# Kernel optimization log

Hardware: AMD Instinct MI355X
Metric: run time of the kernel (lower is better)

The kernel has to match this reference:

```python
import jax, jax.numpy as jnp
import numpy as np

N_NODES = 100000
N_EDGES = 1600000
D_IN = 128
HIDDEN = 128
EPS = 1e-5


def setup_inputs() -> dict:
    key = jax.random.key(0)
    ks = jax.random.split(key, 12)
    glorot = lambda k, o, i: jax.random.normal(k, (o, i), jnp.float32) * (2.0 / (o + i)) ** 0.5
    return {
        "x": jax.random.normal(ks[0], (N_NODES, D_IN), jnp.float32),
        "edge_index": jax.random.randint(ks[1], (2, N_EDGES), 0, N_NODES, jnp.int64),
        # SAGEConv layer 1: lin_l (neighbors, with bias), lin_r (root, no bias)
        "Wl1": glorot(ks[2], HIDDEN, D_IN),
        "bl1": jnp.zeros((HIDDEN,), jnp.float32),
        "Wr1": glorot(ks[3], HIDDEN, D_IN),
        # SAGEConv layer 2
        "Wl2": glorot(ks[4], HIDDEN, HIDDEN),
        "bl2": jnp.zeros((HIDDEN,), jnp.float32),
        "Wr2": glorot(ks[5], HIDDEN, HIDDEN),
        # BatchNorm1d affine params
        "gamma": jnp.ones((HIDDEN,), jnp.float32),
        "beta": jnp.zeros((HIDDEN,), jnp.float32),
        # final fc (xavier_uniform weight, zero bias per init_weights)
        "fcW": jax.random.uniform(ks[6], (HIDDEN, HIDDEN), jnp.float32, -1.0, 1.0) * (6.0 / (2 * HIDDEN)) ** 0.5,
        "fcb": jnp.zeros((HIDDEN,), jnp.float32),
    }


def _sage_conv(h, src, dst, n, Wl, bl, Wr):
    # mean-aggregate neighbor features: scatter x[src] onto dst
    msg_sum = jax.ops.segment_sum(h[src], dst, num_segments=n)          # [N, F]
    deg = jax.ops.segment_sum(jnp.ones((src.shape[0],), h.dtype), dst, num_segments=n)
    agg = msg_sum / jnp.maximum(deg, 1.0)[:, None]
    return agg @ Wl.T + bl + h @ Wr.T


def reference(x, edge_index, Wl1, bl1, Wr1, Wl2, bl2, Wr2, gamma, beta, fcW, fcb):
    src, dst = edge_index[0], edge_index[1]
    n = x.shape[0]
    h = jax.nn.relu(_sage_conv(x, src, dst, n, Wl1, bl1, Wr1))  # inter-layer relu in PyG BasicGNN
    h = _sage_conv(h, src, dst, n, Wl2, bl2, Wr2)
    h = jax.nn.relu(h)
    # BatchNorm1d, training-mode (batch stats, biased variance)
    mu = h.mean(axis=0)
    var = ((h - mu) ** 2).mean(axis=0)
    h = (h - mu) * jax.lax.rsqrt(var + EPS) * gamma + beta
    # dropout p=0.0 -> identity
    return h @ fcW.T + fcb
```

## Files before the change

### kernel.cpp

```cpp
#include <hip/hip_runtime.h>
#include <hip/hip_bf16.h>

#define D 128
#define EPSV 1e-5f
#define BSH 7
#define BWIDTH 128
#define NCB 256
#define MAXBUCK 1024

typedef __attribute__((ext_vector_type(8))) short bf16x8;
typedef __attribute__((ext_vector_type(4))) float f32x4;
typedef unsigned short u16;

__device__ inline u16 f2bf(float f) {
    unsigned int u = __builtin_bit_cast(unsigned int, f);
    return (u16)((u + 0x7fffu + ((u >> 16) & 1u)) >> 16);
}
__device__ inline float bf2f(u16 u) {
    unsigned int x = ((unsigned int)u) << 16;
    return __builtin_bit_cast(float, x);
}

__global__ void k_cvt(const float* __restrict__ in, u16* __restrict__ out, long long n8) {
    long long i = (long long)blockIdx.x * blockDim.x + threadIdx.x;
    long long stride = (long long)gridDim.x * blockDim.x;
    for (; i < n8; i += stride) {
        const float4 v0 = *(const float4*)(in + i * 8);
        const float4 v1 = *(const float4*)(in + i * 8 + 4);
        bf16x8 o;
        o[0] = (short)f2bf(v0.x); o[1] = (short)f2bf(v0.y);
        o[2] = (short)f2bf(v0.z); o[3] = (short)f2bf(v0.w);
        o[4] = (short)f2bf(v1.x); o[5] = (short)f2bf(v1.y);
        o[6] = (short)f2bf(v1.z); o[7] = (short)f2bf(v1.w);
        *(bf16x8*)(out + i * 8) = o;
    }
}

__global__ __launch_bounds__(256) void k_bhist(const int* __restrict__ dst, int E, int chunk,
                                               int nbuck, int* __restrict__ bh) {
    __shared__ int h[MAXBUCK];
    int t = threadIdx.x;
    for (int i = t; i < nbuck; i += 256) h[i] = 0;
    __syncthreads();
    int beg = blockIdx.x * chunk, end = min(E, beg + chunk);
    for (int i = beg + t; i < end; i += 256) atomicAdd(&h[dst[i] >> BSH], 1);
    __syncthreads();
    for (int i = t; i < nbuck; i += 256) bh[(size_t)blockIdx.x * nbuck + i] = h[i];
}

__global__ __launch_bounds__(NCB) void k_colscan(int* __restrict__ bh, int nbuck, int* __restrict__ btot) {
    __shared__ int sm[NCB];
    int b = blockIdx.x;
    int t = threadIdx.x;
    int v = bh[(size_t)t * nbuck + b];
    sm[t] = v;
    __syncthreads();
    for (int off = 1; off < NCB; off <<= 1) {
        int a = (t >= off) ? sm[t - off] : 0;
        __syncthreads();
        sm[t] += a;
        __syncthreads();
    }
    bh[(size_t)t * nbuck + b] = sm[t] - v;
    if (t == NCB - 1) btot[b] = sm[t];
}

__global__ __launch_bounds__(1024) void k_btotscan(const int* __restrict__ btot, int nbuck,
                                                   int* __restrict__ bbase, int* __restrict__ row_ptr,
                                                   int M, int E) {
    __shared__ int sm[1024];
    int t = threadIdx.x;
    int v = (t < nbuck) ? btot[t] : 0;
    sm[t] = v;
    __syncthreads();
    for (int off = 1; off < 1024; off <<= 1) {
        int a = (t >= off) ? sm[t - off] : 0;
        __syncthreads();
        sm[t] += a;
        __syncthreads();
    }
    if (t < nbuck) bbase[t] = sm[t] - v;
    if (t == 0) { bbase[nbuck] = E; row_ptr[M] = E; }
}

__global__ __launch_bounds__(256) void k_bfill(const int* __restrict__ src, const int* __restrict__ dst,
                                               int E, int chunk, int nbuck, const int* __restrict__ bh,
                                               const int* __restrict__ bbase, unsigned int* __restrict__ pairs) {
    __shared__ int cur[MAXBUCK];
    int t = threadIdx.x;
    for (int i = t; i < nbuck; i += 256)
        cur[i] = bbase[i] + bh[(size_t)blockIdx.x * nbuck + i];
    __syncthreads();
    int beg = blockIdx.x * chunk, end = min(E, beg + chunk);
    for (int i = beg + t; i < end; i += 256) {
        int d = dst[i];
        int bk = d >> BSH;
        int pos = atomicAdd(&cur[bk], 1);
        pairs[pos] = (unsigned int)src[i] | ((unsigned int)(d & (BWIDTH - 1)) << 24);
    }
}

__global__ __launch_bounds__(256) void k_b2csr(const unsigned int* __restrict__ pairs,
                                               const int* __restrict__ bbase, int nbuck, int M,
                                               int* __restrict__ row_ptr, int* __restrict__ csr) {
    __shared__ int nh[BWIDTH];
    __shared__ int sc[BWIDTH];
    __shared__ int nc[BWIDTH];
    int b = blockIdx.x;
    int t = threadIdx.x;
    int node0 = b << BSH;
    int beg = bbase[b], end = bbase[b + 1];
    if (t < BWIDTH) nh[t] = 0;
    __syncthreads();
    for (int i = beg + t; i < end; i += 256) atomicAdd(&nh[pairs[i] >> 24], 1);
    __syncthreads();
    if (t < BWIDTH) sc[t] = nh[t];
    __syncthreads();
    for (int off = 1; off < BWIDTH; off <<= 1) {
        int a = 0;
        if (t < BWIDTH && t >= off) a = sc[t - off];
        __syncthreads();
        if (t < BWIDTH) sc[t] += a;
        __syncthreads();
    }
    if (t < BWIDTH) {
        int ex = sc[t] - nh[t];
        nc[t] = ex;
        int node = node0 + t;
        if (node < M) row_ptr[node] = beg + ex;
    }
    __syncthreads();
    for (int i = beg + t; i < end; i += 256) {
        unsigned int p = pairs[i];
        int pos = atomicAdd(&nc[p >> 24], 1);
        csr[beg + pos] = (int)(p & 0xFFFFFFu);
    }
}

__global__ __launch_bounds__(256) void k_gather(const u16* __restrict__ feat, const int* __restrict__ rp,
                                                const int* __restrict__ csr, u16* __restrict__ msg, int M) {
    int sub = threadIdx.x & 15;
    int node = blockIdx.x * 16 + (threadIdx.x >> 4);
    if (node >= M) return;
    int beg = rp[node], end = rp[node + 1];
    float a0[8], a1[8];
    #pragma unroll
    for (int j = 0; j < 8; j++) { a0[j] = 0.f; a1[j] = 0.f; }
    int e = beg;
    for (; e + 1 < end; e += 2) {
        int s0 = csr[e], s1 = csr[e + 1];
        bf16x8 v0 = *(const bf16x8*)(feat + (size_t)s0 * D + sub * 8);
        bf16x8 v1 = *(const bf16x8*)(feat + (size_t)s1 * D + sub * 8);
        #pragma unroll
        for (int j = 0; j < 8; j++) {
            a0[j] += bf2f((u16)v0[j]);
            a1[j] += bf2f((u16)v1[j]);
        }
    }
    if (e < end) {
        bf16x8 v0 = *(const bf16x8*)(feat + (size_t)csr[e] * D + sub * 8);
        #pragma unroll
        for (int j = 0; j < 8; j++) a0[j] += bf2f((u16)v0[j]);
    }
    float inv = 1.0f / fmaxf((float)(end - beg), 1.0f);
    bf16x8 o;
    #pragma unroll
    for (int j = 0; j < 8; j++) o[j] = (short)f2bf((a0[j] + a1[j]) * inv);
    *(bf16x8*)(msg + (size_t)node * D + sub * 8) = o;
}

template <int TWO, int RELU, int OUTBF>
__global__ __launch_bounds__(256) void k_gemm(
    const u16* __restrict__ A1, const u16* __restrict__ A2,
    const u16* __restrict__ W1b, const u16* __restrict__ W2b,
    const float* __restrict__ bias, void* __restrict__ Cout, int M) {
    int lane = threadIdx.x & 63;
    int wave = threadIdx.x >> 6;
    int rlo = lane & 15;
    int k0 = (lane >> 4) * 8;
    int m0 = blockIdx.x * 128 + wave * 32;

    f32x4 acc[2][8];
    #pragma unroll
    for (int mt = 0; mt < 2; mt++)
        #pragma unroll
        for (int nt = 0; nt < 8; nt++) acc[mt][nt] = (f32x4){0.f, 0.f, 0.f, 0.f};

    {
        bf16x8 af[2][4];
        #pragma unroll
        for (int mt = 0; mt < 2; mt++) {
            int ra = m0 + mt * 16 + rlo;
            if (ra > M - 1) ra = M - 1;
            const u16* arow = A1 + (size_t)ra * D;
            #pragma unroll
            for (int kk = 0; kk < 4; kk++)
                af[mt][kk] = *(const bf16x8*)(arow + kk * 32 + k0);
        }
        #pragma unroll
        for (int nt = 0; nt < 8; nt++) {
            const u16* wrow = W1b + (size_t)(nt * 16 + rlo) * D;
            bf16x8 wf[4];
            #pragma unroll
            for (int kk = 0; kk < 4; kk++)
                wf[kk] = *(const bf16x8*)(wrow + kk * 32 + k0);
            #pragma unroll
            for (int mt = 0; mt < 2; mt++)
                #pragma unroll
                for (int kk = 0; kk < 4; kk++)
                    acc[mt][nt] = __builtin_amdgcn_mfma_f32_16x16x32_bf16(af[mt][kk], wf[kk], acc[mt][nt], 0, 0, 0);
        }
    }

    if (TWO) {
        bf16x8 af[2][4];
        #pragma unroll
        for (int mt = 0; mt < 2; mt++) {
            int ra = m0 + mt * 16 + rlo;
            if (ra > M - 1) ra = M - 1;
            const u16* arow = A2 + (size_t)ra * D;
            #pragma unroll
            for (int kk = 0; kk < 4; kk++)
                af[mt][kk] = *(const bf16x8*)(arow + kk * 32 + k0);
        }
        #pragma unroll
        for (int nt = 0; nt < 8; nt++) {
            const u16* wrow = W2b + (size_t)(nt * 16 + rlo) * D;
            bf16x8 wf[4];
            #pragma unroll
            for (int kk = 0; kk < 4; kk++)
                wf[kk] = *(const bf16x8*)(wrow + kk * 32 + k0);
            #pragma unroll
            for (int mt = 0; mt < 2; mt++)
                #pragma unroll
                for (int kk = 0; kk < 4; kk++)
                    acc[mt][nt] = __builtin_amdgcn_mfma_f32_16x16x32_bf16(af[mt][kk], wf[kk], acc[mt][nt], 0, 0, 0);
        }
    }

    #pragma unroll
    for (int mt = 0; mt < 2; mt++)
        #pragma unroll
        for (int nt = 0; nt < 8; nt++) {
            int col = nt * 16 + rlo;
            float bn = bias[col];
            #pragma unroll
            for (int r = 0; r < 4; r++) {
                int row = m0 + mt * 16 + (lane >> 4) * 4 + r;
                if (row < M) {
                    float v = acc[mt][nt][r] + bn;
                    if (RELU) v = fmaxf(v, 0.0f);
                    if (OUTBF) ((u16*)Cout)[(size_t)row * D + col] = f2bf(v);
                    else       ((float*)Cout)[(size_t)row * D + col] = v;
                }
            }
        }
}

__global__ __launch_bounds__(256) void k_bnstats(const u16* __restrict__ h, int M, float* __restrict__ stats) {
    __shared__ float ssum[256];
    __shared__ float ssq[256];
    int col = threadIdx.x & 127;
    int half = threadIdx.x >> 7;
    float s = 0.f, s2 = 0.f;
    for (int r = blockIdx.x * 2 + half; r < M; r += 512) {
        float v = bf2f(h[(size_t)r * D + col]);
        s += v;
        s2 += v * v;
    }
    ssum[threadIdx.x] = s;
    ssq[threadIdx.x] = s2;
    __syncthreads();
    if (threadIdx.x < 128) {
        unsafeAtomicAdd(&stats[col], ssum[threadIdx.x] + ssum[threadIdx.x + 128]);
        unsafeAtomicAdd(&stats[128 + col], ssq[threadIdx.x] + ssq[threadIdx.x + 128]);
    }
}

__global__ __launch_bounds__(128) void k_bnfold(const float* __restrict__ stats,
                                                const float* __restrict__ gamma, const float* __restrict__ beta,
                                                const float* __restrict__ fcW, const float* __restrict__ fcb,
                                                int M, u16* __restrict__ Wfold, float* __restrict__ bias2) {
    __shared__ float sc[128], sh[128];
    int t = threadIdx.x;
    float mu = stats[t] / (float)M;
    float var = stats[128 + t] / (float)M - mu * mu;
    float s = gamma[t] * rsqrtf(var + EPSV);
    sc[t] = s;
    sh[t] = beta[t] - mu * s;
    __syncthreads();
    const float* wrow = fcW + (size_t)t * 128;
    float accv = fcb[t];
    #pragma unroll 4
    for (int k = 0; k < 128; k++) {
        float w = wrow[k];
        Wfold[(size_t)t * 128 + k] = f2bf(w * sc[k]);
        accv += sh[k] * w;
    }
    bias2[t] = accv;
}

static inline size_t alup(size_t x) { return (x + 63) & ~(size_t)63; }

extern "C" void kernel_launch(void* const* d_in, const int* in_sizes, int n_in,
                              void* d_out, int out_size, void* d_ws, size_t ws_size,
                              hipStream_t stream) {
    const float* x   = (const float*)d_in[0];
    const int*   ei  = (const int*)d_in[1];
    const float* Wl1 = (const float*)d_in[2];
    const float* bl1 = (const float*)d_in[3];
    const float* Wr1 = (const float*)d_in[4];
    const float* Wl2 = (const float*)d_in[5];
    const float* bl2 = (const float*)d_in[6];
    const float* Wr2 = (const float*)d_in[7];
    const float* gamma = (const float*)d_in[8];
    const float* beta  = (const float*)d_in[9];
    const float* fcW = (const float*)d_in[10];
    const float* fcb = (const float*)d_in[11];
    float* out = (float*)d_out;

    const int M = in_sizes[0] / D;
    const int E = in_sizes[1] / 2;
    const int* srcI = ei;
    const int* dstI = ei + E;
    const int nbuck = (M + BWIDTH - 1) >> BSH;
    const int chunk = (E + NCB - 1) / NCB;

    char* p = (char*)d_ws;
    u16* xb   = (u16*)p;            p += alup((size_t)M * D * 2);
    u16* msgb = (u16*)p;            p += alup((size_t)M * D * 2);
    u16* h1b  = (u16*)p;            p += alup((size_t)M * D * 2);
    u16* h2b  = (u16*)p;            p += alup((size_t)M * D * 2);
    unsigned int* pairs = (unsigned int*)p; p += alup((size_t)E * 4);
    int* csr  = (int*)p;            p += alup((size_t)E * 4);
    int* row_ptr = (int*)p;         p += alup((size_t)(M + 1) * 4);
    int* bh   = (int*)p;            p += alup((size_t)NCB * nbuck * 4);
    int* btot = (int*)p;            p += alup((size_t)nbuck * 4);
    int* bbase= (int*)p;            p += alup((size_t)(nbuck + 1) * 4);
    float* stats = (float*)p;       p += alup(256 * 4);
    u16* Wl1b = (u16*)p;            p += alup((size_t)D * D * 2);
    u16* Wr1b = (u16*)p;            p += alup((size_t)D * D * 2);
    u16* Wl2b = (u16*)p;            p += alup((size_t)D * D * 2);
    u16* Wr2b = (u16*)p;            p += alup((size_t)D * D * 2);
    u16* Wfoldb = (u16*)p;          p += alup((size_t)D * D * 2);
    float* bias2 = (float*)p;       p += alup(128 * 4);

    const int gemm_grid = (M + 127) / 128;
    const int gather_grid = (M + 15) / 16;
    const long long wn8 = (long long)D * D / 8;

    hipMemsetAsync(stats, 0, 256 * sizeof(float), stream);

    k_cvt<<<2048, 256, 0, stream>>>(x, xb, (long long)M * D / 8);
    k_cvt<<<8, 256, 0, stream>>>(Wl1, Wl1b, wn8);
    k_cvt<<<8, 256, 0, stream>>>(Wr1, Wr1b, wn8);
    k_cvt<<<8, 256, 0, stream>>>(Wl2, Wl2b, wn8);
    k_cvt<<<8, 256, 0, stream>>>(Wr2, Wr2b, wn8);
    k_bhist<<<NCB, 256, 0, stream>>>(dstI, E, chunk, nbuck, bh);
    k_colscan<<<nbuck, NCB, 0, stream>>>(bh, nbuck, btot);
    k_btotscan<<<1, 1024, 0, stream>>>(btot, nbuck, bbase, row_ptr, M, E);
    k_bfill<<<NCB, 256, 0, stream>>>(srcI, dstI, E, chunk, nbuck, bh, bbase, pairs);
    k_b2csr<<<nbuck, 256, 0, stream>>>(pairs, bbase, nbuck, M, row_ptr, csr);

    k_gather<<<gather_grid, 256, 0, stream>>>(xb, row_ptr, csr, msgb, M);
    k_gemm<1, 1, 1><<<gemm_grid, 256, 0, stream>>>(msgb, xb, Wl1b, Wr1b, bl1, h1b, M);

    k_gather<<<gather_grid, 256, 0, stream>>>(h1b, row_ptr, csr, msgb, M);
    k_gemm<1, 1, 1><<<gemm_grid, 256, 0, stream>>>(msgb, h1b, Wl2b, Wr2b, bl2, h2b, M);

    k_bnstats<<<256, 256, 0, stream>>>(h2b, M, stats);
    k_bnfold<<<1, 128, 0, stream>>>(stats, gamma, beta, fcW, fcb, M, Wfoldb, bias2);

    k_gemm<0, 0, 0><<<gemm_grid, 256, 0, stream>>>(h2b, nullptr, Wfoldb, nullptr, bias2, out, M);
}
```

Before: 521.2 us.

## Stage GEMM weights in swizzled LDS with persistent blocks, unroll gather, merge weight conversions

The GEMM kernel now loads the bf16 weight matrices once per block into XOR-swizzled LDS and loops over row strips with a grid capped at 512 blocks, so weight fragments are read from LDS instead of global/L2 for every strip. The neighbor gather is unrolled to four edges in flight to raise memory-level parallelism. The four weight conversion launches are merged into one kernel, and the BN-fold kernel is parallelized across 128 blocks with a tree reduction. The trade-offs are more LDS per block (64KB for the two-matrix variant), which limits occupancy, and more registers in the gather.

```diff
diff --git a/kernel.cpp b/kernel.cpp
--- a/kernel.cpp
+++ b/kernel.cpp
@@ -36,6 +36,23 @@
     }
 }
 
+__global__ __launch_bounds__(256) void k_cvt4(const float* __restrict__ s0, const float* __restrict__ s1,
+                                              const float* __restrict__ s2, const float* __restrict__ s3,
+                                              u16* __restrict__ out) {
+    int i = blockIdx.x * 256 + threadIdx.x;
+    int mat = i >> 11;
+    int off = (i & 2047) * 8;
+    const float* src = (mat == 0) ? s0 : (mat == 1) ? s1 : (mat == 2) ? s2 : s3;
+    const float4 v0 = *(const float4*)(src + off);
+    const float4 v1 = *(const float4*)(src + off + 4);
+    bf16x8 o;
+    o[0] = (short)f2bf(v0.x); o[1] = (short)f2bf(v0.y);
+    o[2] = (short)f2bf(v0.z); o[3] = (short)f2bf(v0.w);
+    o[4] = (short)f2bf(v1.x); o[5] = (short)f2bf(v1.y);
+    o[6] = (short)f2bf(v1.z); o[7] = (short)f2bf(v1.w);
+    *(bf16x8*)(out + (size_t)i * 8) = o;
+}
+
 __global__ __launch_bounds__(256) void k_bhist(const int* __restrict__ dst, int E, int chunk,
                                                int nbuck, int* __restrict__ bh) {
     __shared__ int h[MAXBUCK];
@@ -143,21 +160,25 @@
     int node = blockIdx.x * 16 + (threadIdx.x >> 4);
     if (node >= M) return;
     int beg = rp[node], end = rp[node + 1];
-    float a0[8], a1[8];
+    float a0[8], a1[8], a2[8], a3[8];
     #pragma unroll
-    for (int j = 0; j < 8; j++) { a0[j] = 0.f; a1[j] = 0.f; }
+    for (int j = 0; j < 8; j++) { a0[j] = 0.f; a1[j] = 0.f; a2[j] = 0.f; a3[j] = 0.f; }
     int e = beg;
-    for (; e + 1 < end; e += 2) {
-        int s0 = csr[e], s1 = csr[e + 1];
+    for (; e + 3 < end; e += 4) {
+        int s0 = csr[e], s1 = csr[e + 1], s2 = csr[e + 2], s3 = csr[e + 3];
         bf16x8 v0 = *(const bf16x8*)(feat + (size_t)s0 * D + sub * 8);
         bf16x8 v1 = *(const bf16x8*)(feat + (size_t)s1 * D + sub * 8);
+        bf16x8 v2 = *(const bf16x8*)(feat + (size_t)s2 * D + sub * 8);
+        bf16x8 v3 = *(const bf16x8*)(feat + (size_t)s3 * D + sub * 8);
         #pragma unroll
         for (int j = 0; j < 8; j++) {
             a0[j] += bf2f((u16)v0[j]);
             a1[j] += bf2f((u16)v1[j]);
+            a2[j] += bf2f((u16)v2[j]);
+            a3[j] += bf2f((u16)v3[j]);
         }
     }
-    if (e < end) {
+    for (; e < end; e++) {
         bf16x8 v0 = *(const bf16x8*)(feat + (size_t)csr[e] * D + sub * 8);
         #pragma unroll
         for (int j = 0; j < 8; j++) a0[j] += bf2f((u16)v0[j]);
@@ -165,7 +186,7 @@
     float inv = 1.0f / fmaxf((float)(end - beg), 1.0f);
     bf16x8 o;
     #pragma unroll
-    for (int j = 0; j < 8; j++) o[j] = (short)f2bf((a0[j] + a1[j]) * inv);
+    for (int j = 0; j < 8; j++) o[j] = (short)f2bf((a0[j] + a1[j] + a2[j] + a3[j]) * inv);
     *(bf16x8*)(msg + (size_t)node * D + sub * 8) = o;
 }
 
@@ -173,88 +194,98 @@
 __global__ __launch_bounds__(256) void k_gemm(
     const u16* __restrict__ A1, const u16* __restrict__ A2,
     const u16* __restrict__ W1b, const u16* __restrict__ W2b,
-    const float* __restrict__ bias, void* __restrict__ Cout, int M) {
-    int lane = threadIdx.x & 63;
-    int wave = threadIdx.x >> 6;
-    int rlo = lane & 15;
-    int k0 = (lane >> 4) * 8;
-    int m0 = blockIdx.x * 128 + wave * 32;
-
-    f32x4 acc[2][8];
-    #pragma unroll
-    for (int mt = 0; mt < 2; mt++)
-        #pragma unroll
-        for (int nt = 0; nt < 8; nt++) acc[mt][nt] = (f32x4){0.f, 0.f, 0.f, 0.f};
-
+    const float* __restrict__ bias, void* __restrict__ Cout,
+    int M, int nstrips) {
+    __shared__ u16 wlds[(TWO ? 2 : 1) * 16384];
+    int t = threadIdx.x;
     {
-        bf16x8 af[2][4];
+        const int nrows = TWO ? 256 : 128;
+        for (int idx = t; idx < nrows; idx += 256) {
+            int mat = idx >> 7, row = idx & 127;
+            const u16* g = (mat ? W2b : W1b) + (size_t)row * D;
+            u16* base = wlds + mat * 16384 + row * D;
+            #pragma unroll
+            for (int c16 = 0; c16 < 16; c16++) {
+                bf16x8 v = *(const bf16x8*)(g + c16 * 8);
+                *(bf16x8*)(base + ((c16 ^ (row & 7)) * 8)) = v;
+            }
+        }
+    }
+    __syncthreads();
+
+    int lane = t & 63, wave = t >> 6;
+    int rlo = lane & 15, khi = lane >> 4;
+
+    for (int s = blockIdx.x; s < nstrips; s += gridDim.x) {
+        int m0 = s * 128 + wave * 32;
+        bf16x8 a1f[2][4], a2f[2][4];
         #pragma unroll
         for (int mt = 0; mt < 2; mt++) {
             int ra = m0 + mt * 16 + rlo;
             if (ra > M - 1) ra = M - 1;
-            const u16* arow = A1 + (size_t)ra * D;
+            const u16* ar = A1 + (size_t)ra * D;
             #pragma unroll
             for (int kk = 0; kk < 4; kk++)
-                af[mt][kk] = *(const bf16x8*)(arow + kk * 32 + k0);
+                a1f[mt][kk] = *(const bf16x8*)(ar + kk * 32 + khi * 8);
+            if (TWO) {
+                const u16* ar2 = A2 + (size_t)ra * D;
+                #pragma unroll
+                for (int kk = 0; kk < 4; kk++)
+                    a2f[mt][kk] = *(const bf16x8*)(ar2 + kk * 32 + khi * 8);
+            }
         }
+
+        f32x4 acc[2][8];
+        #pragma unroll
+        for (int mt = 0; mt < 2; mt++)
+            #pragma unroll
+            for (int nt = 0; nt < 8; nt++) acc[mt][nt] = (f32x4){0.f, 0.f, 0.f, 0.f};
+
         #pragma unroll
         for (int nt = 0; nt < 8; nt++) {
-            const u16* wrow = W1b + (size_t)(nt * 16 + rlo) * D;
+            int row = nt * 16 + rlo;
+            const u16* wb = wlds + (size_t)row * D;
             bf16x8 wf[4];
             #pragma unroll
             for (int kk = 0; kk < 4; kk++)
-                wf[kk] = *(const bf16x8*)(wrow + kk * 32 + k0);
+                wf[kk] = *(const bf16x8*)(wb + ((kk * 4 + khi) ^ (row & 7)) * 8);
             #pragma unroll
             for (int mt = 0; mt < 2; mt++)
                 #pragma unroll
                 for (int kk = 0; kk < 4; kk++)
-                    acc[mt][nt] = __builtin_amdgcn_mfma_f32_16x16x32_bf16(af[mt][kk], wf[kk], acc[mt][nt], 0, 0, 0);
-        }
-    }
-
-    if (TWO) {
-        bf16x8 af[2][4];
-        #pragma unroll
-        for (int mt = 0; mt < 2; mt++) {
-            int ra = m0 + mt * 16 + rlo;
-            if (ra > M - 1) ra = M - 1;
-            const u16* arow = A2 + (size_t)ra * D;
-            #pragma unroll
-            for (int kk = 0; kk < 4; kk++)
-                af[mt][kk] = *(const bf16x8*)(arow + kk * 32 + k0);
-        }
-        #pragma unroll
-        for (int nt = 0; nt < 8; nt++) {
-            const u16* wrow = W2b + (size_t)(nt * 16 + rlo) * D;
-            bf16x8 wf[4];
-            #pragma unroll
-            for (int kk = 0; kk < 4; kk++)
-                wf[kk] = *(const bf16x8*)(wrow + kk * 32 + k0);
-            #pragma unroll
-            for (int mt = 0; mt < 2; mt++)
+                    acc[mt][nt] = __builtin_amdgcn_mfma_f32_16x16x32_bf16(a1f[mt][kk], wf[kk], acc[mt][nt], 0, 0, 0);
+            if (TWO) {
+                const u16* wb2 = wlds + 16384 + (size_t)row * D;
+                bf16x8 wf2[4];
                 #pragma unroll
                 for (int kk = 0; kk < 4; kk++)
-                    acc[mt][nt] = __builtin_amdgcn_mfma_f32_16x16x32_bf16(af[mt][kk], wf[kk], acc[mt][nt], 0, 0, 0);
+                    wf2[kk] = *(const bf16x8*)(wb2 + ((kk * 4 + khi) ^ (row & 7)) * 8);
+                #pragma unroll
+                for (int mt = 0; mt < 2; mt++)
+                    #pragma unroll
+                    for (int kk = 0; kk < 4; kk++)
+                        acc[mt][nt] = __builtin_amdgcn_mfma_f32_16x16x32_bf16(a2f[mt][kk], wf2[kk], acc[mt][nt], 0, 0, 0);
+            }
         }
-    }
-
-    #pragma unroll
-    for (int mt = 0; mt < 2; mt++)
-        #pragma unroll
-        for (int nt = 0; nt < 8; nt++) {
-            int col = nt * 16 + rlo;
-            float bn = bias[col];
-            #pragma unroll
-            for (int r = 0; r < 4; r++) {
-                int row = m0 + mt * 16 + (lane >> 4) * 4 + r;
-                if (row < M) {
-                    float v = acc[mt][nt][r] + bn;
-                    if (RELU) v = fmaxf(v, 0.0f);
-                    if (OUTBF) ((u16*)Cout)[(size_t)row * D + col] = f2bf(v);
-                    else       ((float*)Cout)[(size_t)row * D + col] = v;
+
+        #pragma unroll
+        for (int mt = 0; mt < 2; mt++)
+            #pragma unroll
+            for (int nt = 0; nt < 8; nt++) {
+                int col = nt * 16 + rlo;
+                float bn = bias[col];
+                #pragma unroll
+                for (int r = 0; r < 4; r++) {
+                    int row = m0 + mt * 16 + khi * 4 + r;
+                    if (row < M) {
+                        float v = acc[mt][nt][r] + bn;
+                        if (RELU) v = fmaxf(v, 0.0f);
+                        if (OUTBF) ((u16*)Cout)[(size_t)row * D + col] = f2bf(v);
+                        else       ((float*)Cout)[(size_t)row * D + col] = v;
+                    }
                 }
             }
-        }
+    }
 }
 
 __global__ __launch_bounds__(256) void k_bnstats(const u16* __restrict__ h, int M, float* __restrict__ stats) {
@@ -281,23 +312,21 @@
                                                 const float* __restrict__ gamma, const float* __restrict__ beta,
                                                 const float* __restrict__ fcW, const float* __restrict__ fcb,
                                                 int M, u16* __restrict__ Wfold, float* __restrict__ bias2) {
-    __shared__ float sc[128], sh[128];
-    int t = threadIdx.x;
+    __shared__ float red[128];
+    int n = blockIdx.x, t = threadIdx.x;
     float mu = stats[t] / (float)M;
     float var = stats[128 + t] / (float)M - mu * mu;
-    float s = gamma[t] * rsqrtf(var + EPSV);
-    sc[t] = s;
-    sh[t] = beta[t] - mu * s;
-    __syncthreads();
-    const float* wrow = fcW + (size_t)t * 128;
-    float accv = fcb[t];
-    #pragma unroll 4
-    for (int k = 0; k < 128; k++) {
-        float w = wrow[k];
-        Wfold[(size_t)t * 128 + k] = f2bf(w * sc[k]);
-        accv += sh[k] * w;
-    }
-    bias2[t] = accv;
+    float sc = gamma[t] * rsqrtf(var + EPSV);
+    float sh = beta[t] - mu * sc;
+    float w = fcW[(size_t)n * D + t];
+    Wfold[(size_t)n * D + t] = f2bf(w * sc);
+    red[t] = sh * w;
+    __syncthreads();
+    for (int off = 64; off > 0; off >>= 1) {
+        if (t < off) red[t] += red[t + off];
+        __syncthreads();
+    }
+    if (t == 0) bias2[n] = fcb[n] + red[0];
 }
 
 static inline size_t alup(size_t x) { return (x + 63) & ~(size_t)63; }
@@ -338,24 +367,23 @@
     int* btot = (int*)p;            p += alup((size_t)nbuck * 4);
     int* bbase= (int*)p;            p += alup((size_t)(nbuck + 1) * 4);
     float* stats = (float*)p;       p += alup(256 * 4);
-    u16* Wl1b = (u16*)p;            p += alup((size_t)D * D * 2);
-    u16* Wr1b = (u16*)p;            p += alup((size_t)D * D * 2);
-    u16* Wl2b = (u16*)p;            p += alup((size_t)D * D * 2);
-    u16* Wr2b = (u16*)p;            p += alup((size_t)D * D * 2);
+    u16* Wb   = (u16*)p;            p += alup((size_t)4 * D * D * 2);
     u16* Wfoldb = (u16*)p;          p += alup((size_t)D * D * 2);
     float* bias2 = (float*)p;       p += alup(128 * 4);
 
-    const int gemm_grid = (M + 127) / 128;
+    u16* Wl1b = Wb;
+    u16* Wr1b = Wb + 16384;
+    u16* Wl2b = Wb + 32768;
+    u16* Wr2b = Wb + 49152;
+
+    const int nstrips = (M + 127) / 128;
+    const int GG = nstrips < 512 ? nstrips : 512;
     const int gather_grid = (M + 15) / 16;
-    const long long wn8 = (long long)D * D / 8;
 
     hipMemsetAsync(stats, 0, 256 * sizeof(float), stream);
 
     k_cvt<<<2048, 256, 0, stream>>>(x, xb, (long long)M * D / 8);
-    k_cvt<<<8, 256, 0, stream>>>(Wl1, Wl1b, wn8);
-    k_cvt<<<8, 256, 0, stream>>>(Wr1, Wr1b, wn8);
-    k_cvt<<<8, 256, 0, stream>>>(Wl2, Wl2b, wn8);
-    k_cvt<<<8, 256, 0, stream>>>(Wr2, Wr2b, wn8);
+    k_cvt4<<<32, 256, 0, stream>>>(Wl1, Wr1, Wl2, Wr2, Wb);
     k_bhist<<<NCB, 256, 0, stream>>>(dstI, E, chunk, nbuck, bh);
     k_colscan<<<nbuck, NCB, 0, stream>>>(bh, nbuck, btot);
     k_btotscan<<<1, 1024, 0, stream>>>(btot, nbuck, bbase, row_ptr, M, E);
@@ -363,13 +391,13 @@
     k_b2csr<<<nbuck, 256, 0, stream>>>(pairs, bbase, nbuck, M, row_ptr, csr);
 
     k_gather<<<gather_grid, 256, 0, stream>>>(xb, row_ptr, csr, msgb, M);
-    k_gemm<1, 1, 1><<<gemm_grid, 256, 0, stream>>>(msgb, xb, Wl1b, Wr1b, bl1, h1b, M);
+    k_gemm<1, 1, 1><<<GG, 256, 0, stream>>>(msgb, xb, Wl1b, Wr1b, bl1, h1b, M, nstrips);
 
     k_gather<<<gather_grid, 256, 0, stream>>>(h1b, row_ptr, csr, msgb, M);
-    k_gemm<1, 1, 1><<<gemm_grid, 256, 0, stream>>>(msgb, h1b, Wl2b, Wr2b, bl2, h2b, M);
+    k_gemm<1, 1, 1><<<GG, 256, 0, stream>>>(msgb, h1b, Wl2b, Wr2b, bl2, h2b, M, nstrips);
 
     k_bnstats<<<256, 256, 0, stream>>>(h2b, M, stats);
-    k_bnfold<<<1, 128, 0, stream>>>(stats, gamma, beta, fcW, fcb, M, Wfoldb, bias2);
-
-    k_gemm<0, 0, 0><<<gemm_grid, 256, 0, stream>>>(h2b, nullptr, Wfoldb, nullptr, bias2, out, M);
-}
+    k_bnfold<<<128, 128, 0, stream>>>(stats, gamma, beta, fcW, fcb, M, Wfoldb, bias2);
+
+    k_gemm<0, 0, 0><<<GG, 256, 0, stream>>>(h2b, nullptr, Wfoldb, nullptr, bias2, out, M, nstrips);
+}
```

New measurement: 451.5 us. -13.4%, faster.
